# Optimization experiments

Measured on AMD Instinct MI355X. Metric: run time of the kernel, lower is better.

Reference implementation:

```python
import jax, jax.numpy as jnp
import numpy as np

# Default widths from CWT.__init__: round((exp(linspace(0,2.5,5))-1)*30)+1
WIDTHS = [1, 27, 76, 167, 336]


def _morlet_int_psi():
    """pywt 'morl' wavelet: psi(t)=exp(-t^2/2)*cos(5t) on [-8,8], precision=10,
    integrated (cumulative) as in pywt.integrate_wavelet."""
    precision = 10
    n = 2 ** precision
    lb, ub = -8.0, 8.0
    t = np.linspace(lb, ub, n)
    psi = np.exp(-t ** 2 / 2.0) * np.cos(5.0 * t)
    step = t[1] - t[0]
    int_psi = np.cumsum(psi) * step
    return int_psi, step, lb, ub, n


def _filters(widths):
    """Per-scale resampled integrated wavelet, as in pywt.cwt.
    pywt uses np.convolve(data, int_psi[j][::-1]) (which flips its kernel);
    lax conv is a correlation (no flip), so the equivalent lax kernel is int_psi[j]."""
    int_psi, step, lb, ub, n = _morlet_int_psi()
    filts = []
    for scale in widths:
        j = (np.arange(scale * (ub - lb) + 1) / (scale * step)).astype(np.int64)
        j = j[j < n]
        filts.append(int_psi[j].astype(np.float32))
    return filts

_FILTERS = _filters(WIDTHS)


def _cwt_forward(x):
    # x: [N, T, C]; conv along T, channels independent
    N, T, C = x.shape
    xt = x.transpose(0, 2, 1).reshape(N * C, 1, T)  # [N*C, 1, T]
    outs = []
    for scale, f in zip(WIDTHS, _FILTERS):
        L = f.shape[0]
        k = jnp.asarray(f)[None, None, :]  # [out=1, in=1, L]
        # 'full' convolution: pad L-1 on each side
        conv = jax.lax.conv_general_dilated(xt, k, window_strides=(1,), padding=[(L - 1, L - 1)])  # [N*C,1,T+L-1]
        coef = (-np.sqrt(float(scale))) * jnp.diff(conv, axis=-1)  # [N*C,1,T+L-2]
        d = (coef.shape[-1] - T) / 2.0  # trim to central T samples (pywt)
        lo = int(np.floor(d))
        hi = coef.shape[-1] - int(np.ceil(d))
        coef = coef[..., lo:hi]  # [N*C, 1, T]
        outs.append(coef.reshape(N, C, T))
    out = jnp.stack(outs, axis=0)  # [F, N, C, T]
    return out.transpose(1, 3, 2, 0)  # [N, T, C, F]


def setup_inputs() -> dict:
    key = jax.random.key(0)
    x = jax.random.normal(key, (16, 2048, 64), dtype=jnp.float32)
    return {"x": x}


def reference(x):
    return _cwt_forward(x)
```

## Files before the change

kernel.cpp:

```cpp
#include <hip/hip_runtime.h>
#include <hip/hip_fp16.h>
#include <math.h>

#define NB    16
#define T     2048
#define NC    64
#define NROWS (NB*NC)
#define PADL2 2696
#define XSH_N 7440
#define XSH_PAD 7568


#define WS_XT    655360u
#define WS_OUTT  4849664u

typedef _Float16 half8  __attribute__((ext_vector_type(8)));
typedef _Float16 half4v __attribute__((ext_vector_type(4)));
typedef float    f32x16 __attribute__((ext_vector_type(16)));

__global__ __launch_bounds__(1024) void cwt_prep(const float* __restrict__ x,
                                                 __half* __restrict__ xT,
                                                 __half* __restrict__ W) {
    __shared__ double ps[1024];
    __shared__ double sc[1024];
    __shared__ float  k32[1024];
    __shared__ float  tile4[4][64 * 65];
    const int tid = threadIdx.x;

    if (blockIdx.x < 32) {
        const int bb = blockIdx.x;
        constexpr int SCe[5]    = {336, 167, 76, 27, 1};
        constexpr int KS16[5]   = {5424, 2720, 1264, 480, 64};
        constexpr int WOFF32[5] = {0, 173568, 260608, 301056, 316416};
        constexpr int CLO16[5]  = {0, 84, 130, 154, 167};

        {
            const uint4 z = make_uint4(0u, 0u, 0u, 0u);
            #pragma unroll
            for (int sl = 0; sl < 5; ++sl) {
                uint4* z4 = (uint4*)(W + WOFF32[sl] + bb * KS16[sl]);
                const int n8 = KS16[sl] / 8;
                for (int i = tid; i < n8; i += 1024) z4[i] = z;
            }
        }

        const double delta = 16.0 / 1023.0;
        double t = (tid == 1023) ? 8.0 : (-8.0 + delta * (double)tid);
        {
            const float tf = (float)t;
            ps[tid] = (double)(expf(-0.5f * tf * tf) * cosf(5.0f * tf));
        }
        __syncthreads();

        double* a = ps; double* b = sc;
        for (int off = 1; off < 1024; off <<= 1) {
            double v = a[tid];
            if (tid >= off) v += a[tid - off];
            b[tid] = v;
            __syncthreads();
            double* tmp = a; a = b; b = tmp;
        }
        const double step = ((-8.0 + delta) + 8.0);
        k32[tid] = (float)(a[tid] * step);
        __syncthreads();

        for (int sl = 0; sl < 5; ++sl) {
            const int s = SCe[sl];
            const int L = 16 * s + 1;
            const double c = (double)s * step;
            const float sq = (float)sqrt((double)s);
            const int posoff = PADL2 - 8 * s - 1;
            const int kb0 = posoff - 16 * CLO16[sl];
            __half* wb = W + WOFF32[sl] + bb * KS16[sl];
            for (int i = tid; i <= L; i += 1024) {
                float g; bool wr = true;
                if (i == 0) {
                    g = sq * k32[0];
                } else if (i == L) {
                    long long jl = (long long)((double)(L - 1) / c);
                    if (jl > 1023) jl = 1023;
                    g = -sq * k32[jl];
                } else {
                    long long j1 = (long long)((double)i / c);
                    long long j0 = (long long)((double)(i - 1) / c);
                    if (j1 > 1023) j1 = 1023;
                    if (j0 > 1023) j0 = 1023;
                    wr = (j1 > j0);
                    g = sq * (k32[j1] - k32[j0]);
                }
                if (wr) {
                    wb[kb0 + i + bb] = __float2half(g);
                }
            }
        }
    } else {
        const int g    = tid >> 8;
        const int t256 = tid & 255;
        const int ti   = (blockIdx.x - 32) * 4 + g;
        const int n    = ti >> 5;
        const int t0   = (ti & 31) << 6;
        float* tl = tile4[g];

        const float4* src = (const float4*)(x + ((size_t)(n * T + t0)) * NC);
        #pragma unroll
        for (int k = 0; k < 4; ++k) {
            float4 v = src[t256 + 256 * k];
            const int flat = (t256 + 256 * k) * 4;
            const int tt = flat >> 6, c = flat & 63;
            tl[tt * 65 + c + 0] = v.x;
            tl[tt * 65 + c + 1] = v.y;
            tl[tt * 65 + c + 2] = v.z;
            tl[tt * 65 + c + 3] = v.w;
        }
        __syncthreads();
        const int lane = t256 & 63, w4 = t256 >> 6;
        for (int cc = w4; cc < 64; cc += 4) {
            xT[((size_t)(n * 64 + cc)) * T + t0 + lane] = __float2half(tl[lane * 65 + cc]);
        }
    }
}

template<int N, int DEPTH>
__device__ __forceinline__ void conv_seg(int c0, int c1,
                                         const _Float16* __restrict__ xb0,
                                         const _Float16* __restrict__ xb1,
                                         const _Float16* const (&ap)[5],
                                         f32x16 (&acc)[5][2]) {
    half8 A[DEPTH][N];
    half8 B0[DEPTH], B1[DEPTH];
    #pragma unroll
    for (int d = 0; d < DEPTH; ++d) {
        const int ko = (c0 + d) << 4;
        #pragma unroll
        for (int sl = 0; sl < N; ++sl) A[d][sl] = *(const half8*)(ap[sl] + ko);
        B0[d] = *(const half8*)(xb0 + ko);
        B1[d] = *(const half8*)(xb1 + ko);
    }
    int c = c0;
    for (; c + DEPTH <= c1; c += DEPTH) {
        #pragma unroll
        for (int d = 0; d < DEPTH; ++d) {
            #pragma unroll
            for (int sl = 0; sl < N; ++sl) {
                acc[sl][0] = __builtin_amdgcn_mfma_f32_32x32x16_f16(A[d][sl], B0[d], acc[sl][0], 0, 0, 0);
                acc[sl][1] = __builtin_amdgcn_mfma_f32_32x32x16_f16(A[d][sl], B1[d], acc[sl][1], 0, 0, 0);
            }
            const int ko = (c + DEPTH + d) << 4;
            #pragma unroll
            for (int sl = 0; sl < N; ++sl) A[d][sl] = *(const half8*)(ap[sl] + ko);
            B0[d] = *(const half8*)(xb0 + ko);
            B1[d] = *(const half8*)(xb1 + ko);
        }
    }
    #pragma unroll
    for (int d = 0; d < DEPTH; ++d) {
        if (d < c1 - c) {
            #pragma unroll
            for (int sl = 0; sl < N; ++sl) {
                acc[sl][0] = __builtin_amdgcn_mfma_f32_32x32x16_f16(A[d][sl], B0[d], acc[sl][0], 0, 0, 0);
                acc[sl][1] = __builtin_amdgcn_mfma_f32_32x32x16_f16(A[d][sl], B1[d], acc[sl][1], 0, 0, 0);
            }
        }
    }
}

__global__ __launch_bounds__(128, 1) void cwt_conv_mfma(const __half* __restrict__ xT,
                                                        const __half* __restrict__ Wg,
                                                        __half* __restrict__ outT) {
    constexpr int KS16[5]   = {5424, 2720, 1264, 480, 64};
    constexpr int WOFF32[5] = {0, 173568, 260608, 301056, 316416};
    constexpr int CLO16[5]  = {0, 84, 130, 154, 167};
    constexpr int OS[5]     = {4, 3, 2, 1, 0};

    __shared__ _Float16 xsh[2][XSH_PAD];
    __shared__ _Float16 ostage[2048];
    const int tid  = threadIdx.x;
    const int rp   = blockIdx.x;
    const int lane = tid & 63;
    const int w    = tid >> 6;
    const int col  = lane & 31;
    const int kh   = lane >> 5;

    {
        const uint4 z = make_uint4(0u, 0u, 0u, 0u);
        #pragma unroll
        for (int rr = 0; rr < 2; ++rr) {
            uint4* x4 = (uint4*)xsh[rr];
            for (int i = tid; i < XSH_N / 8; i += 128)
                if (i < PADL2 / 8 || i >= (PADL2 + T) / 8) x4[i] = z;
            const uint4* src = (const uint4*)(xT + (size_t)(2 * rp + rr) * T);
            x4[PADL2 / 8 + tid] = src[tid];
            x4[PADL2 / 8 + 128 + tid] = src[128 + tid];
        }
    }
    __syncthreads();

    const _Float16* xb0 = xsh[0] + 32 * (32 * w + col) + 8 * kh;
    const _Float16* xb1 = xsh[1] + 32 * (32 * w + col) + 8 * kh;
    const _Float16* ap[5];
    #pragma unroll
    for (int sl = 0; sl < 5; ++sl)
        ap[sl] = (const _Float16*)Wg + WOFF32[sl] + col * KS16[sl] + 8 * kh
                 - 16 * CLO16[sl];

    f32x16 acc[5][2];
    #pragma unroll
    for (int sl = 0; sl < 5; ++sl)
        #pragma unroll
        for (int rr = 0; rr < 2; ++rr)
            #pragma unroll
            for (int r = 0; r < 16; ++r) acc[sl][rr][r] = 0.f;

    conv_seg<1,4>(  0,  84, xb0, xb1, ap, acc);
    conv_seg<2,3>( 84, 130, xb0, xb1, ap, acc);
    conv_seg<3,2>(130, 154, xb0, xb1, ap, acc);
    conv_seg<4,2>(154, 167, xb0, xb1, ap, acc);
    conv_seg<5,1>(167, 171, xb0, xb1, ap, acc);
    conv_seg<4,2>(171, 184, xb0, xb1, ap, acc);
    conv_seg<3,2>(184, 209, xb0, xb1, ap, acc);
    conv_seg<2,3>(209, 254, xb0, xb1, ap, acc);
    conv_seg<1,4>(254, 339, xb0, xb1, ap, acc);

    _Float16* os = ostage + 1024 * w;
    #pragma unroll
    for (int rr = 0; rr < 2; ++rr) {
        const int row  = 2 * rp + rr;
        const int nidx = row >> 6;
        const int cidx = row & 63;
        #pragma unroll
        for (int sl = 0; sl < 5; ++sl) {
            #pragma unroll
            for (int rq = 0; rq < 4; ++rq) {
                half4v hv;
                #pragma unroll
                for (int r = 0; r < 4; ++r) hv[r] = (_Float16)acc[sl][rr][4 * rq + r];
                *(half4v*)(os + 32 * col + 8 * rq + 4 * kh) = hv;
            }
            half8 o0 = *(const half8*)(os + 16 * lane);
            half8 o1 = *(const half8*)(os + 16 * lane + 8);
            __half* ob = outT + ((size_t)(((nidx * 128 + 64 * w + lane) * 64 + cidx) * 5 + OS[sl])) * 16;
            *(half8*)(ob)     = o0;
            *(half8*)(ob + 8) = o1;
        }
    }
}

__global__ __launch_bounds__(256) void cwt_fix(const __half* __restrict__ outT,
                                               float* __restrict__ out) {
    __shared__ float tile[16 * 320];
    const int b  = blockIdx.x;
    const int n  = b >> 7;
    const int tb = b & 127;
    const int tid = threadIdx.x;

    const uint4* src = (const uint4*)(outT + (size_t)(n * 128 + tb) * 5120);
    for (int i = tid; i < 640; i += 256) {
        uint4 v = src[i];
        const __half* h = (const __half*)&v;
        const int h0  = i * 8;
        const int sg  = h0 >> 4;
        const int tt0 = h0 & 15;
        #pragma unroll
        for (int k = 0; k < 8; ++k) tile[(tt0 + k) * 320 + sg] = __half2float(h[k]);
    }
    __syncthreads();
    float4* dst = (float4*)(out + (size_t)(n * 2048 + tb * 16) * 320);
    const float4* tl = (const float4*)tile;
    for (int k = tid; k < 1280; k += 256) dst[k] = tl[k];
}

extern "C" void kernel_launch(void* const* d_in, const int* in_sizes, int n_in,
                              void* d_out, int out_size, void* d_ws, size_t ws_size,
                              hipStream_t stream) {
    const float* x = (const float*)d_in[0];
    float* out = (float*)d_out;
    char* ws = (char*)d_ws;

    __half* W    = (__half*)ws;
    __half* xT   = (__half*)(ws + WS_XT);
    __half* outT = (__half*)(ws + WS_OUTT);

    cwt_prep<<<160, 1024, 0, stream>>>(x, xT, W);
    cwt_conv_mfma<<<NROWS / 2, 128, 0, stream>>>(xT, W, outT);
    cwt_fix<<<2048, 256, 0, stream>>>(outT, out);
}
```

Before: 144.8 us.

## Split MFMA K-range across wave pairs with LDS reduction and padded shared layout

Doubles the conv block to four waves: two wave pairs each cover half of the K-chunk range (by segment), then the second pair's accumulators are reduced into the first through LDS over four rounds. The shared input buffer gets a padded layout (one extra 16-byte unit every 32) to cut LDS bank conflicts on the B-operand loads. The aim is more parallelism per block and better latency hiding with two blocks per CU. In exchange it adds a reduction with eight barriers, extra LDS usage, and register pressure under the 256-thread, 2-block launch bound.

```diff
diff --git a/kernel.cpp b/kernel.cpp
--- a/kernel.cpp
+++ b/kernel.cpp
@@ -8,8 +8,11 @@
 #define NROWS (NB*NC)
 #define PADL2 2696
 #define XSH_N 7440
-#define XSH_PAD 7568
-
+
+
+#define PU(u) ((u) + ((u) >> 5))
+#define XSH_UNITS 930
+#define XSH_PHYSH 7808
 
 #define WS_XT    655360u
 #define WS_OUTT  4849664u
@@ -121,9 +124,9 @@
 }
 
 template<int N, int DEPTH>
-__device__ __forceinline__ void conv_seg(int c0, int c1,
-                                         const _Float16* __restrict__ xb0,
-                                         const _Float16* __restrict__ xb1,
+__device__ __forceinline__ void conv_seg(int c0, int c1, int blu,
+                                         const _Float16* __restrict__ xs0,
+                                         const _Float16* __restrict__ xs1,
                                          const _Float16* const (&ap)[5],
                                          f32x16 (&acc)[5][2]) {
     half8 A[DEPTH][N];
@@ -133,8 +136,9 @@
         const int ko = (c0 + d) << 4;
         #pragma unroll
         for (int sl = 0; sl < N; ++sl) A[d][sl] = *(const half8*)(ap[sl] + ko);
-        B0[d] = *(const half8*)(xb0 + ko);
-        B1[d] = *(const half8*)(xb1 + ko);
+        const int lu = blu + 2 * (c0 + d);
+        B0[d] = *(const half8*)(xs0 + 8 * PU(lu));
+        B1[d] = *(const half8*)(xs1 + 8 * PU(lu));
     }
     int c = c0;
     for (; c + DEPTH <= c1; c += DEPTH) {
@@ -148,8 +152,9 @@
             const int ko = (c + DEPTH + d) << 4;
             #pragma unroll
             for (int sl = 0; sl < N; ++sl) A[d][sl] = *(const half8*)(ap[sl] + ko);
-            B0[d] = *(const half8*)(xb0 + ko);
-            B1[d] = *(const half8*)(xb1 + ko);
+            const int lu = blu + 2 * (c + DEPTH + d);
+            B0[d] = *(const half8*)(xs0 + 8 * PU(lu));
+            B1[d] = *(const half8*)(xs1 + 8 * PU(lu));
         }
     }
     #pragma unroll
@@ -164,7 +169,7 @@
     }
 }
 
-__global__ __launch_bounds__(128, 1) void cwt_conv_mfma(const __half* __restrict__ xT,
+__global__ __launch_bounds__(256, 2) void cwt_conv_mfma(const __half* __restrict__ xT,
                                                         const __half* __restrict__ Wg,
                                                         __half* __restrict__ outT) {
     constexpr int KS16[5]   = {5424, 2720, 1264, 480, 64};
@@ -172,31 +177,32 @@
     constexpr int CLO16[5]  = {0, 84, 130, 154, 167};
     constexpr int OS[5]     = {4, 3, 2, 1, 0};
 
-    __shared__ _Float16 xsh[2][XSH_PAD];
+    __shared__ _Float16 xsh[2][XSH_PHYSH];
     __shared__ _Float16 ostage[2048];
+    __shared__ float    red[2][2][1088];
     const int tid  = threadIdx.x;
     const int rp   = blockIdx.x;
     const int lane = tid & 63;
-    const int w    = tid >> 6;
+    const int wv   = tid >> 6;
+    const int wh   = wv & 1;
+    const int wp   = wv >> 1;
     const int col  = lane & 31;
     const int kh   = lane >> 5;
 
     {
         const uint4 z = make_uint4(0u, 0u, 0u, 0u);
-        #pragma unroll
-        for (int rr = 0; rr < 2; ++rr) {
-            uint4* x4 = (uint4*)xsh[rr];
-            for (int i = tid; i < XSH_N / 8; i += 128)
-                if (i < PADL2 / 8 || i >= (PADL2 + T) / 8) x4[i] = z;
-            const uint4* src = (const uint4*)(xT + (size_t)(2 * rp + rr) * T);
-            x4[PADL2 / 8 + tid] = src[tid];
-            x4[PADL2 / 8 + 128 + tid] = src[128 + tid];
+        for (int ii = tid; ii < 2 * XSH_UNITS; ii += 256) {
+            const int rr = (ii >= XSH_UNITS) ? 1 : 0;
+            const int i  = ii - XSH_UNITS * rr;
+            uint4 v = z;
+            if (i >= PADL2 / 8 && i < (PADL2 + T) / 8)
+                v = ((const uint4*)(xT + (size_t)(2 * rp + rr) * T))[i - PADL2 / 8];
+            ((uint4*)xsh[rr])[PU(i)] = v;
         }
     }
     __syncthreads();
 
-    const _Float16* xb0 = xsh[0] + 32 * (32 * w + col) + 8 * kh;
-    const _Float16* xb1 = xsh[1] + 32 * (32 * w + col) + 8 * kh;
+    const int blu = 128 * wh + 4 * col + kh;
     const _Float16* ap[5];
     #pragma unroll
     for (int sl = 0; sl < 5; ++sl)
@@ -211,36 +217,66 @@
             #pragma unroll
             for (int r = 0; r < 16; ++r) acc[sl][rr][r] = 0.f;
 
-    conv_seg<1,4>(  0,  84, xb0, xb1, ap, acc);
-    conv_seg<2,3>( 84, 130, xb0, xb1, ap, acc);
-    conv_seg<3,2>(130, 154, xb0, xb1, ap, acc);
-    conv_seg<4,2>(154, 167, xb0, xb1, ap, acc);
-    conv_seg<5,1>(167, 171, xb0, xb1, ap, acc);
-    conv_seg<4,2>(171, 184, xb0, xb1, ap, acc);
-    conv_seg<3,2>(184, 209, xb0, xb1, ap, acc);
-    conv_seg<2,3>(209, 254, xb0, xb1, ap, acc);
-    conv_seg<1,4>(254, 339, xb0, xb1, ap, acc);
-
-    _Float16* os = ostage + 1024 * w;
-    #pragma unroll
-    for (int rr = 0; rr < 2; ++rr) {
-        const int row  = 2 * rp + rr;
-        const int nidx = row >> 6;
-        const int cidx = row & 63;
-        #pragma unroll
-        for (int sl = 0; sl < 5; ++sl) {
-            #pragma unroll
-            for (int rq = 0; rq < 4; ++rq) {
-                half4v hv;
+    if (wp == 0) {
+        conv_seg<1,4>(  0,  84, blu, xsh[0], xsh[1], ap, acc);
+        conv_seg<2,3>( 84, 130, blu, xsh[0], xsh[1], ap, acc);
+        conv_seg<3,2>(130, 154, blu, xsh[0], xsh[1], ap, acc);
+        conv_seg<4,2>(154, 167, blu, xsh[0], xsh[1], ap, acc);
+        conv_seg<5,1>(167, 171, blu, xsh[0], xsh[1], ap, acc);
+    } else {
+        conv_seg<4,2>(171, 184, blu, xsh[0], xsh[1], ap, acc);
+        conv_seg<3,2>(184, 209, blu, xsh[0], xsh[1], ap, acc);
+        conv_seg<2,3>(209, 254, blu, xsh[0], xsh[1], ap, acc);
+        conv_seg<1,4>(254, 339, blu, xsh[0], xsh[1], ap, acc);
+    }
+
+    __syncthreads();
+    #pragma unroll
+    for (int rnd = 0; rnd < 4; ++rnd) {
+        if (wp == 1) {
+            #pragma unroll
+            for (int j = 0; j < 2; ++j) {
+                const int s2 = rnd * 2 + j, sl = s2 >> 1, rr = s2 & 1;
                 #pragma unroll
-                for (int r = 0; r < 4; ++r) hv[r] = (_Float16)acc[sl][rr][4 * rq + r];
-                *(half4v*)(os + 32 * col + 8 * rq + 4 * kh) = hv;
-            }
-            half8 o0 = *(const half8*)(os + 16 * lane);
-            half8 o1 = *(const half8*)(os + 16 * lane + 8);
-            __half* ob = outT + ((size_t)(((nidx * 128 + 64 * w + lane) * 64 + cidx) * 5 + OS[sl])) * 16;
-            *(half8*)(ob)     = o0;
-            *(half8*)(ob + 8) = o1;
+                for (int r = 0; r < 16; ++r)
+                    red[j][wh][lane * 17 + r] = acc[sl][rr][r];
+            }
+        }
+        __syncthreads();
+        if (wp == 0) {
+            #pragma unroll
+            for (int j = 0; j < 2; ++j) {
+                const int s2 = rnd * 2 + j, sl = s2 >> 1, rr = s2 & 1;
+                #pragma unroll
+                for (int r = 0; r < 16; ++r)
+                    acc[sl][rr][r] += red[j][wh][lane * 17 + r];
+            }
+        }
+        __syncthreads();
+    }
+
+    if (wp == 0) {
+        _Float16* os = ostage + 1024 * wh;
+        #pragma unroll
+        for (int rr = 0; rr < 2; ++rr) {
+            const int row  = 2 * rp + rr;
+            const int nidx = row >> 6;
+            const int cidx = row & 63;
+            #pragma unroll
+            for (int sl = 0; sl < 5; ++sl) {
+                #pragma unroll
+                for (int rq = 0; rq < 4; ++rq) {
+                    half4v hv;
+                    #pragma unroll
+                    for (int r = 0; r < 4; ++r) hv[r] = (_Float16)acc[sl][rr][4 * rq + r];
+                    *(half4v*)(os + 32 * col + 8 * rq + 4 * kh) = hv;
+                }
+                half8 o0 = *(const half8*)(os + 16 * lane);
+                half8 o1 = *(const half8*)(os + 16 * lane + 8);
+                __half* ob = outT + ((size_t)(((nidx * 128 + 64 * wh + lane) * 64 + cidx) * 5 + OS[sl])) * 16;
+                *(half8*)(ob)     = o0;
+                *(half8*)(ob + 8) = o1;
+            }
         }
     }
 }
@@ -281,6 +317,6 @@
     __half* outT = (__half*)(ws + WS_OUTT);
 
     cwt_prep<<<160, 1024, 0, stream>>>(x, xT, W);
-    cwt_conv_mfma<<<NROWS / 2, 128, 0, stream>>>(xT, W, outT);
+    cwt_conv_mfma<<<NROWS / 2, 256, 0, stream>>>(xT, W, outT);
     cwt_fix<<<2048, 256, 0, stream>>>(outT, out);
 }
```

Result: no change. 147.3 us (+1.7%).
